# Kernel optimization log

Measured on AMD Instinct MI355X. Metric: run time of the kernel, lower is better.

## Reference

```python
import jax, jax.numpy as jnp
import numpy as np

N = 128       # SSM state size
L = 32768     # l_max / sequence length
DT_MIN, DT_MAX = 0.001, 0.1


def setup_inputs() -> dict:
    key = jax.random.key(0)
    ku, ka, kb, kc, ks = jax.random.split(key, 5)
    u = jax.random.normal(ku, (L,), dtype=jnp.float32)
    # lecun_normal: std = 1/sqrt(fan_in); shift A by -2I for stability over L powers
    A = jax.random.normal(ka, (N, N), dtype=jnp.float32) * (1.0 / np.sqrt(N)) - 2.0 * jnp.eye(N, dtype=jnp.float32)
    B = jax.random.normal(kb, (N, 1), dtype=jnp.float32)            # fan_in=1 -> std 1
    C = jax.random.normal(kc, (1, N), dtype=jnp.float32) * (1.0 / np.sqrt(N))
    D = jnp.ones((1,), dtype=jnp.float32)
    log_step = jax.random.uniform(ks, (1,), dtype=jnp.float32) * (np.log(DT_MAX) - np.log(DT_MIN)) + np.log(DT_MIN)
    return {"u": u, "A": A, "B": B, "C": C, "D": D, "log_step": log_step}


def discretize(a, b, step):
    # bilinear (Tustin) discretization, identical to the flax module
    i = jnp.eye(a.shape[0], dtype=a.dtype)
    bl = jnp.linalg.inv(i - (step / 2.0) * a)
    ab = bl @ (i + (step / 2.0) * a)
    bb = (bl * step) @ b
    return ab, bb


def k_conv(ab, bb, cb, l):
    # K[t] = cb @ ab^t @ bb  -- same math as the matrix_power list-comp,
    # computed with a single scan carrying x_t = ab^t @ bb  (N,1)
    def step(x, _):
        k_t = (cb @ x).reshape(())
        return ab @ x, k_t
    _, k = jax.lax.scan(step, bb, None, length=l)
    return k  # (l,)


def causal_convolution(u, k):
    l = u.shape[0]
    ud = jnp.fft.rfft(jnp.pad(u, (0, k.shape[0])))
    kd = jnp.fft.rfft(jnp.pad(k, (0, l)))
    return jnp.fft.irfft(ud * kd)[:l]


def reference(u, A, B, C, D, log_step):
    step = jnp.exp(log_step)
    ab, bb = discretize(A, B, step)
    K = k_conv(ab, bb, C, u.shape[0])
    return causal_convolution(u, K) + D * u
```

## Files before the change

### kernel.cpp

```cpp
#include <hip/hip_runtime.h>
#include <math.h>

#define L_SEQ 32768
#define PL 16384
#define PLG 32768

typedef unsigned short u16;
typedef float f32x4 __attribute__((ext_vector_type(4)));
typedef short bf16x8 __attribute__((ext_vector_type(8)));
typedef u16 u16x4 __attribute__((ext_vector_type(4)));

__device__ __forceinline__ u16 f2bf(float x) {
  unsigned u = __float_as_uint(x);
  u = u + 0x7FFFu + ((u >> 16) & 1u);
  return (u16)(u >> 16);
}
__device__ __forceinline__ float bf2f(u16 h) { return __uint_as_float(((unsigned)h) << 16); }
__device__ __forceinline__ int MIDX(int r, int c) { return (r << 7) + (c ^ ((r & 7) << 3)); }
__device__ __forceinline__ f32x4 MF(bf16x8 a, bf16x8 b, f32x4 c) {
  return __builtin_amdgcn_mfma_f32_16x16x32_bf16(a, b, c, 0, 0, 0);
}
__device__ __forceinline__ void gfrag(const u16* g, int row, int kp, bf16x8& h, bf16x8& l) {
  h = *(const bf16x8*)(g + row * 128 + kp);
  l = *(const bf16x8*)(g + PLG + row * 128 + kp);
}
__device__ __forceinline__ void lfrag(const u16* base, int row, int kp, bf16x8& h, bf16x8& l) {
  h = *(const bf16x8*)(base + MIDX(row, kp));
  l = *(const bf16x8*)(base + PL + MIDX(row, kp));
}
__device__ __forceinline__ void pack4(const float* v, u16x4& hi, u16x4& lo) {
#pragma unroll
  for (int j = 0; j < 4; ++j) {
    u16 h = f2bf(v[j]);
    hi[j] = h;
    lo[j] = f2bf(v[j] - bf2f(h));
  }
}

template<int MK, int ERS, bool HEC, bool M2, bool DUMP>
__device__ void step(u16* lds,
                     const u16* gAm, const u16* gU, float c3, u16* gDump,
                     int ER, const u16* gAe, u16* gOe, int eR0,
                     const u16* gT1, const u16* gT2x,
                     int EC, const u16* gBe, u16* gOc, int eC0) {
  u16* Mb = lds;
  u16* Tb = lds + 2 * PL;
  const int t = threadIdx.x, lane = t & 63, la = lane & 15, g = lane >> 4;
  const int w = t >> 6, wr = w >> 2, wc = w & 3;
  const int r0 = wr << 5, c0 = wc << 5;
  constexpr int ERN = (ERS > 0) ? ERS : 1;

  __syncthreads();

  f32x4 acc[2][2], accT[2][2], accE[ERN][2], accC[2][2];
#pragma unroll
  for (int i = 0; i < 2; ++i)
#pragma unroll
    for (int j = 0; j < 2; ++j) {
      acc[i][j] = (f32x4){0.f, 0.f, 0.f, 0.f};
      accT[i][j] = (f32x4){0.f, 0.f, 0.f, 0.f};
      accC[i][j] = (f32x4){0.f, 0.f, 0.f, 0.f};
    }
#pragma unroll
  for (int f = 0; f < ERN; ++f)
#pragma unroll
    for (int j = 0; j < 2; ++j) accE[f][j] = (f32x4){0.f, 0.f, 0.f, 0.f};

#pragma unroll
  for (int kb = 0; kb < 4; ++kb) {
    const int kp = (kb << 5) + (g << 3);
    bf16x8 Ah[2], Al[2], Bh[2], Bl[2];
    if constexpr (MK != 0) {
#pragma unroll
      for (int fr = 0; fr < 2; ++fr) {
        int ar = r0 + (fr << 4) + la;
        if constexpr (MK == 1) lfrag(Mb, ar, kp, Ah[fr], Al[fr]);
        else gfrag(gAm, ar, kp, Ah[fr], Al[fr]);
      }
    }
#pragma unroll
    for (int fc = 0; fc < 2; ++fc) {
      int bc = c0 + (fc << 4) + la;
      lfrag(Tb, bc, kp, Bh[fc], Bl[fc]);
    }
    bf16x8 Eh[ERN], El[ERN];
    if constexpr (ERS > 0) {
#pragma unroll
      for (int f = 0; f < ERS; ++f) {
        int er = (wr << 4) + (f << 6) + la;
        gfrag(gAe, er, kp, Eh[f], El[f]);
      }
    }
    bf16x8 Fh[2], Fl[2];
    if constexpr (HEC) {
#pragma unroll
      for (int e = 0; e < 2; ++e) {
        int ec = (wc << 5) + (e << 4) + la;
        gfrag(gBe, ec, kp, Fh[e], Fl[e]);
      }
    }
    if constexpr (MK != 0) {
#pragma unroll
      for (int fr = 0; fr < 2; ++fr)
#pragma unroll
        for (int fc = 0; fc < 2; ++fc) {
          acc[fr][fc] = MF(Ah[fr], Bh[fc], acc[fr][fc]);
          acc[fr][fc] = MF(Ah[fr], Bl[fc], acc[fr][fc]);
          acc[fr][fc] = MF(Al[fr], Bh[fc], acc[fr][fc]);
          accT[fr][fc] = MF(Bh[fc], Ah[fr], accT[fr][fc]);
          accT[fr][fc] = MF(Bh[fc], Al[fr], accT[fr][fc]);
          accT[fr][fc] = MF(Bl[fc], Ah[fr], accT[fr][fc]);
        }
    }
    if constexpr (ERS > 0) {
#pragma unroll
      for (int f = 0; f < ERS; ++f)
#pragma unroll
        for (int fc = 0; fc < 2; ++fc) {
          accE[f][fc] = MF(Bh[fc], Eh[f], accE[f][fc]);
          accE[f][fc] = MF(Bh[fc], El[f], accE[f][fc]);
          accE[f][fc] = MF(Bl[fc], Eh[f], accE[f][fc]);
        }
    }
    if constexpr (HEC) {
#pragma unroll
      for (int fr = 0; fr < 2; ++fr)
#pragma unroll
        for (int e = 0; e < 2; ++e) {
          accC[fr][e] = MF(Ah[fr], Fh[e], accC[fr][e]);
          accC[fr][e] = MF(Ah[fr], Fl[e], accC[fr][e]);
          accC[fr][e] = MF(Al[fr], Fh[e], accC[fr][e]);
        }
    }
  }

  __syncthreads();

  if constexpr (MK != 0) {
#pragma unroll
    for (int fr = 0; fr < 2; ++fr)
#pragma unroll
      for (int fc = 0; fc < 2; ++fc) {
        int rr = r0 + (fr << 4) + la;
        int cb = c0 + (fc << 4) + (g << 2);
        float v[4];
#pragma unroll
        for (int j = 0; j < 4; ++j) v[j] = accT[fr][fc][j];
        if constexpr (MK == 2) {
#pragma unroll
          for (int j = 0; j < 4; ++j)
            v[j] = c3 * (v[j] + bf2f(gU[rr * 128 + cb + j]) +
                         bf2f(gU[PLG + rr * 128 + cb + j])) -
                   ((rr == cb + j) ? 1.f : 0.f);
        }
        u16x4 hi, lo;
        pack4(v, hi, lo);
        *(u16x4*)(Mb + MIDX(rr, cb)) = hi;
        *(u16x4*)(Mb + PL + MIDX(rr, cb)) = lo;
        if constexpr (DUMP) {
          *(u16x4*)(gDump + rr * 128 + cb) = hi;
          *(u16x4*)(gDump + PLG + rr * 128 + cb) = lo;
        }
        int cc = c0 + (fc << 4) + la;
        int rb = r0 + (fr << 4) + (g << 2);
        float q[4];
#pragma unroll
        for (int j = 0; j < 4; ++j) q[j] = acc[fr][fc][j];
        if constexpr (MK == 2) {
#pragma unroll
          for (int j = 0; j < 4; ++j)
            q[j] = c3 * (q[j] + bf2f(gU[(rb + j) * 128 + cc]) +
                         bf2f(gU[PLG + (rb + j) * 128 + cc])) -
                   ((rb + j == cc) ? 1.f : 0.f);
        }
        u16x4 hi2, lo2;
        pack4(q, hi2, lo2);
        *(u16x4*)(Tb + MIDX(cc, rb)) = hi2;
        *(u16x4*)(Tb + PL + MIDX(cc, rb)) = lo2;
      }
  }
  if constexpr (ERS > 0) {
#pragma unroll
    for (int f = 0; f < ERS; ++f) {
      int er = (wr << 4) + (f << 6) + la;
      if (er < ER) {
#pragma unroll
        for (int fc = 0; fc < 2; ++fc) {
          int cb = c0 + (fc << 4) + (g << 2);
          float v[4];
#pragma unroll
          for (int j = 0; j < 4; ++j) v[j] = accE[f][fc][j];
          if constexpr (M2) {
            u16x4 t1h = *(const u16x4*)(gT1 + er * 128 + cb);
            u16x4 t1l = *(const u16x4*)(gT1 + PLG + er * 128 + cb);
            u16x4 t2h = *(const u16x4*)(gT2x + er * 128 + cb);
            u16x4 t2l = *(const u16x4*)(gT2x + PLG + er * 128 + cb);
#pragma unroll
            for (int j = 0; j < 4; ++j)
              v[j] += bf2f(t1h[j]) + bf2f(t1l[j]) + bf2f(t2h[j]) + bf2f(t2l[j]) +
                      ((er == cb + j) ? 1.f : 0.f);
          }
          u16x4 hi, lo;
          pack4(v, hi, lo);
          *(u16x4*)(gOe + (eR0 + er) * 128 + cb) = hi;
          *(u16x4*)(gOe + PLG + (eR0 + er) * 128 + cb) = lo;
        }
      }
    }
  }
  if constexpr (HEC) {
#pragma unroll
    for (int e = 0; e < 2; ++e) {
      int ec = (wc << 5) + (e << 4) + la;
      if (ec < EC) {
#pragma unroll
        for (int fr = 0; fr < 2; ++fr) {
          int rb = r0 + (fr << 4) + (g << 2);
          float v[4];
#pragma unroll
          for (int j = 0; j < 4; ++j) v[j] = accC[fr][e][j];
          u16x4 hi, lo;
          pack4(v, hi, lo);
          *(u16x4*)(gOc + (eC0 + ec) * 128 + rb) = hi;
          *(u16x4*)(gOc + PLG + (eC0 + ec) * 128 + rb) = lo;
        }
      }
    }
  }
}

__global__ void __launch_bounds__(1024)
__attribute__((amdgpu_waves_per_eu(1, 4)))
chain_k(const float* __restrict__ A, const float* __restrict__ Bv,
        const float* __restrict__ Cv, const float* __restrict__ lstep,
        u16* ws) {
  extern __shared__ u16 lds[];
  const int bid = blockIdx.x;
  u16* gT  = ws + bid * 98304;
  u16* gT2 = gT + 32768;
  u16* gU  = gT + 65536;
  u16* rt  = ws + 196608;
  u16* gs  = ws + 262144;

  const int t = threadIdx.x;
  const float stp = expf(lstep[0]);
  const float alpha = 0.5f * stp / (1.f + stp);
  const float c3 = 2.f / (1.f + stp);
  u16* Mh = lds; u16* Ml = lds + PL; u16* Th = lds + 2 * PL; u16* Tl = lds + 3 * PL;

#pragma unroll
  for (int i = 0; i < 4; ++i) {
    int e4 = (t + (i << 10)) << 2;
    int r = e4 >> 7, c = e4 & 127;
    float4 av = *(const float4*)(A + e4);
    float vv[4] = {av.x, av.y, av.z, av.w};
    float tv[4];
#pragma unroll
    for (int j = 0; j < 4; ++j) tv[j] = alpha * (vv[j] + ((r == c + j) ? 2.f : 0.f));
    u16x4 hi, lo;
    pack4(tv, hi, lo);
    *(u16x4*)(Mh + MIDX(r, c)) = hi;
    *(u16x4*)(Ml + MIDX(r, c)) = lo;
    *(u16x4*)(gT + r * 128 + c) = hi;
    *(u16x4*)(gT + PLG + r * 128 + c) = lo;
#pragma unroll
    for (int j = 0; j < 4; ++j) {
      Th[MIDX(c + j, r)] = hi[j];
      Tl[MIDX(c + j, r)] = lo[j];
    }
  }

  step<1,0,false,false,true>(lds, 0, 0, 0.f, gT2,
                             0, 0, 0, 0, 0, 0, 0, 0, 0, 0);
  step<1,2,false,true,false>(lds, 0, 0, 0.f, 0,
                             128, gT, gU, 0, gT, gT2, 0, 0, 0, 0);
  step<2,0,false,false,false>(lds, gU, gU, c3, 0,
                              0, 0, 0, 0, 0, 0, 0, 0, 0, 0);

  if (bid == 0) {
    __syncthreads();
    if (t < 128) {
      float a2 = 0.f;
      for (int p = 0; p < 128; ++p)
        a2 = fmaf(bf2f(Mh[MIDX(t, p)]) + bf2f(Ml[MIDX(t, p)]), Bv[p], a2);
      float v = 0.5f * stp * (a2 + Bv[t]);
      u16 h = f2bf(v);
      rt[t] = h;
      rt[PLG + t] = f2bf(v - bf2f(h));
    }
    for (int i = 1; i <= 8; ++i) {
      int EC = 1 << (i - 1);
      step<1,0,true,false,false>(lds, 0, 0, 0.f, 0,
                                 0, 0, 0, 0, 0, 0, EC, rt, rt, EC);
    }
  } else {
    __syncthreads();
    if (t < 128) {
      float v = Cv[t];
      u16 h = f2bf(v);
      gs[t] = h;
      gs[PLG + t] = f2bf(v - bf2f(h));
    }
    for (int i = 1; i <= 8; ++i)
      step<1,0,false,false,false>(lds, 0, 0, 0.f, 0,
                                  0, 0, 0, 0, 0, 0, 0, 0, 0, 0);
    for (int j = 0; j <= 5; ++j) {
      int ER = 1 << j;
      step<1,1,false,false,false>(lds, 0, 0, 0.f, 0,
                                  ER, gs, gs, ER, 0, 0, 0, 0, 0, 0);
    }
    step<0,1,false,false,false>(lds, 0, 0, 0.f, 0,
                                64, gs, gs, 64, 0, 0, 0, 0, 0, 0);
  }
}

__global__ __launch_bounds__(256) void kmat_k(const u16* __restrict__ gs,
                                              const u16* __restrict__ rt,
                                              float* __restrict__ Kv) {
  __shared__ float srow[128];
  int t1 = blockIdx.x, t0 = threadIdx.x;
  if (t0 < 128)
    srow[t0] = bf2f(gs[t1 * 128 + t0]) + bf2f(gs[PLG + t1 * 128 + t0]);
  __syncthreads();
  const u16* rh = rt + t0 * 128;
  const u16* rl = rt + PLG + t0 * 128;
  float acc = 0.f;
#pragma unroll 4
  for (int p = 0; p < 128; p += 8) {
    uint4 qh = *(const uint4*)(rh + p);
    uint4 ql = *(const uint4*)(rl + p);
    unsigned dh[4] = {qh.x, qh.y, qh.z, qh.w};
    unsigned dl[4] = {ql.x, ql.y, ql.z, ql.w};
#pragma unroll
    for (int j = 0; j < 4; ++j) {
      acc = fmaf(srow[p + 2 * j],     bf2f((u16)dh[j]) + bf2f((u16)dl[j]), acc);
      acc = fmaf(srow[p + 2 * j + 1],
                 bf2f((u16)(dh[j] >> 16)) + bf2f((u16)(dl[j] >> 16)), acc);
    }
  }
  Kv[t1 * 256 + t0] = acc;
}

__global__ __launch_bounds__(64) void conv_k(const float* __restrict__ u,
                                             const float* __restrict__ Kv,
                                             float* __restrict__ Pp) {
  __shared__ __align__(16) float ks[512];
  __shared__ __align__(16) float usw[1536];

  int bid = blockIdx.x, tid = threadIdx.x;
  int m = (int)((sqrtf(4.f * (float)bid + 1.f) - 1.f) * 0.5f);
  while ((m + 1) * (m + 2) <= bid) ++m;
  while (m * (m + 1) > bid) --m;
  int j = bid - m * (m + 1);
  int w0 = (m << 10) - (j << 9) - 512;

  for (int idx = tid; idx < 512; idx += 64) ks[idx] = Kv[(j << 9) + idx];
  for (int idx = tid; idx < 1536; idx += 64) {
    int gi = w0 + idx;
    float v = (gi >= 0) ? u[gi] : 0.f;
    int b = idx >> 2, pb = b ^ ((b >> 3) & 7);
    usw[(pb << 2) | (idx & 3)] = v;
  }
  __syncthreads();

  int tb = tid << 4;
  float acc[16];
#pragma unroll
  for (int z = 0; z < 16; ++z) acc[z] = 0.f;

#define LD4(x) (*(const float4*)&usw[((((x) >> 2) ^ ((((x) >> 2) >> 3) & 7)) << 2)])
  float wf[20];
  {
    float4 a0 = LD4(508 + tb), a1 = LD4(512 + tb), a2 = LD4(516 + tb),
           a3 = LD4(520 + tb), a4 = LD4(524 + tb);
    wf[0] = a0.x; wf[1] = a0.y; wf[2] = a0.z; wf[3] = a0.w;
    wf[4] = a1.x; wf[5] = a1.y; wf[6] = a1.z; wf[7] = a1.w;
    wf[8] = a2.x; wf[9] = a2.y; wf[10] = a2.z; wf[11] = a2.w;
    wf[12] = a3.x; wf[13] = a3.y; wf[14] = a3.z; wf[15] = a3.w;
    wf[16] = a4.x; wf[17] = a4.y; wf[18] = a4.z; wf[19] = a4.w;
  }
  for (int q = 0; q < 512; q += 4) {
    float4 k4 = *(const float4*)&ks[q];
    float kk[4] = {k4.x, k4.y, k4.z, k4.w};
#pragma unroll
    for (int ds = 0; ds < 4; ++ds)
#pragma unroll
      for (int oi = 0; oi < 16; ++oi)
        acc[oi] = fmaf(kk[ds], wf[oi - ds + 4], acc[oi]);
    if (q < 508) {
#pragma unroll
      for (int z = 19; z >= 4; --z) wf[z] = wf[z - 4];
      float4 nw = LD4(504 + tb - q);
      wf[0] = nw.x; wf[1] = nw.y; wf[2] = nw.z; wf[3] = nw.w;
    }
  }
#undef LD4

  float* dst = Pp + (bid << 10) + tb;
#pragma unroll
  for (int z = 0; z < 16; z += 4)
    *(float4*)(dst + z) = make_float4(acc[z], acc[z + 1], acc[z + 2], acc[z + 3]);
}

__global__ __launch_bounds__(256) void reduce_k(const float* __restrict__ Pp,
                                                const float* __restrict__ u,
                                                const float* __restrict__ D,
                                                float* __restrict__ y) {
  int t = blockIdx.x * 256 + threadIdx.x;
  if (t >= L_SEQ) return;
  int m = t >> 10;
  int nJ = 2 * (m + 1);
  const float* base = Pp + ((m * (m + 1)) << 10) + (t & 1023);
  float acc = D[0] * u[t];
  for (int j = 0; j < nJ; ++j) acc += base[j << 10];
  y[t] = acc;
}

extern "C" void kernel_launch(void* const* d_in, const int* in_sizes, int n_in,
                              void* d_out, int out_size, void* d_ws, size_t ws_size,
                              hipStream_t stream) {
  (void)in_sizes; (void)n_in; (void)out_size; (void)ws_size;
  const float* u     = (const float*)d_in[0];
  const float* A     = (const float*)d_in[1];
  const float* B     = (const float*)d_in[2];
  const float* C     = (const float*)d_in[3];
  const float* D     = (const float*)d_in[4];
  const float* lstep = (const float*)d_in[5];
  float* y = (float*)d_out;
  u16* ws = (u16*)d_ws;

  u16* rt = ws + 196608;
  u16* gs = ws + 262144;
  float* Kv = (float*)((char*)d_ws + 622592);
  float* Pp = (float*)((char*)d_ws + 753664);

  (void)hipFuncSetAttribute((const void*)chain_k,
                            hipFuncAttributeMaxDynamicSharedMemorySize, 131072);
  hipLaunchKernelGGL(chain_k, dim3(2), dim3(1024), 131072, stream, A, B, C, lstep, ws);
  hipLaunchKernelGGL(kmat_k, dim3(128), dim3(256), 0, stream, gs, rt, Kv);
  hipLaunchKernelGGL(conv_k, dim3(1056), dim3(64), 0, stream, u, Kv, Pp);
  hipLaunchKernelGGL(reduce_k, dim3(L_SEQ / 256), dim3(256), 0, stream, Pp, u, D, y);
}
```

Before: 236.7 us.

## Split matrix-power chain into producer block and two flag-synchronised consumer blocks

Before, two blocks each redundantly computed the Cayley inverse and the power chain, and each then ran its own doubling steps serially. Now one producer block computes the powers of the discretised matrix once and publishes each one to a global slot behind a release flag. Two consumer blocks spin on those flags and build the K-vector row and column tables as soon as each power is ready, so the doubling work overlaps with the chain. This adds inter-block spin-wait synchronisation, coherent atomic loads and stores, and a memset, and it assumes all three blocks are co-resident or it could deadlock.

Result: slower. 304.9 us (+28.8%).

```diff
diff --git a/kernel.cpp b/kernel.cpp
--- a/kernel.cpp
+++ b/kernel.cpp
@@ -2,8 +2,8 @@
 #include <math.h>
 
 #define L_SEQ 32768
-#define PL 16384
-#define PLG 32768
+#define PL  16384
+#define GPL 16384
 
 typedef unsigned short u16;
 typedef float f32x4 __attribute__((ext_vector_type(4)));
@@ -20,14 +20,6 @@
 __device__ __forceinline__ f32x4 MF(bf16x8 a, bf16x8 b, f32x4 c) {
   return __builtin_amdgcn_mfma_f32_16x16x32_bf16(a, b, c, 0, 0, 0);
 }
-__device__ __forceinline__ void gfrag(const u16* g, int row, int kp, bf16x8& h, bf16x8& l) {
-  h = *(const bf16x8*)(g + row * 128 + kp);
-  l = *(const bf16x8*)(g + PLG + row * 128 + kp);
-}
-__device__ __forceinline__ void lfrag(const u16* base, int row, int kp, bf16x8& h, bf16x8& l) {
-  h = *(const bf16x8*)(base + MIDX(row, kp));
-  l = *(const bf16x8*)(base + PL + MIDX(row, kp));
-}
 __device__ __forceinline__ void pack4(const float* v, u16x4& hi, u16x4& lo) {
 #pragma unroll
   for (int j = 0; j < 4; ++j) {
@@ -36,13 +28,52 @@
     lo[j] = f2bf(v[j] - bf2f(h));
   }
 }
-
-template<int MK, int ERS, bool HEC, bool M2, bool DUMP>
-__device__ void step(u16* lds,
-                     const u16* gAm, const u16* gU, float c3, u16* gDump,
-                     int ER, const u16* gAe, u16* gOe, int eR0,
-                     const u16* gT1, const u16* gT2x,
-                     int EC, const u16* gBe, u16* gOc, int eC0) {
+__device__ __forceinline__ void gfragP(const u16* g, int pl, int row, int kp,
+                                       bf16x8& h, bf16x8& l) {
+  h = *(const bf16x8*)(g + row * 128 + kp);
+  l = *(const bf16x8*)(g + pl + row * 128 + kp);
+}
+__device__ __forceinline__ bf16x8 cohld16(const u16* p) {
+  unsigned long long a = __hip_atomic_load((const unsigned long long*)p,
+                                           __ATOMIC_RELAXED, __HIP_MEMORY_SCOPE_AGENT);
+  unsigned long long b = __hip_atomic_load((const unsigned long long*)p + 1,
+                                           __ATOMIC_RELAXED, __HIP_MEMORY_SCOPE_AGENT);
+  union { unsigned long long x[2]; bf16x8 v; } u;
+  u.x[0] = a; u.x[1] = b;
+  return u.v;
+}
+__device__ __forceinline__ void gfragC(const u16* g, int row, int kp,
+                                       bf16x8& h, bf16x8& l) {
+  h = cohld16(g + row * 128 + kp);
+  l = cohld16(g + GPL + row * 128 + kp);
+}
+__device__ __forceinline__ void cohst8(u16* p, u16x4 v) {
+  union { u16x4 s; unsigned long long x; } u;
+  u.s = v;
+  __hip_atomic_store((unsigned long long*)p, u.x, __ATOMIC_RELAXED,
+                     __HIP_MEMORY_SCOPE_AGENT);
+}
+__device__ __forceinline__ void waitflag(int* f) {
+  if (threadIdx.x == 0) {
+    int it = 0;
+    while (__hip_atomic_load(f, __ATOMIC_ACQUIRE, __HIP_MEMORY_SCOPE_AGENT) == 0 &&
+           it < (1 << 28)) {
+      __builtin_amdgcn_s_sleep(8);
+      ++it;
+    }
+  }
+  __syncthreads();
+}
+__device__ __forceinline__ void setflag(int* f) {
+  __syncthreads();
+  if (threadIdx.x == 0)
+    __hip_atomic_store(f, 1, __ATOMIC_RELEASE, __HIP_MEMORY_SCOPE_AGENT);
+}
+
+template<int MK, int DMP, int ERS, bool M2>
+__device__ void prod_step(u16* lds, const u16* gA, const u16* gU, float c3,
+                          u16* gd, const u16* gAe, u16* gOe,
+                          const u16* gT1, const u16* gT2x) {
   u16* Mb = lds;
   u16* Tb = lds + 2 * PL;
   const int t = threadIdx.x, lane = t & 63, la = lane & 15, g = lane >> 4;
@@ -52,14 +83,13 @@
 
   __syncthreads();
 
-  f32x4 acc[2][2], accT[2][2], accE[ERN][2], accC[2][2];
+  f32x4 acc[2][2], accT[2][2], accE[ERN][2];
 #pragma unroll
   for (int i = 0; i < 2; ++i)
 #pragma unroll
     for (int j = 0; j < 2; ++j) {
       acc[i][j] = (f32x4){0.f, 0.f, 0.f, 0.f};
       accT[i][j] = (f32x4){0.f, 0.f, 0.f, 0.f};
-      accC[i][j] = (f32x4){0.f, 0.f, 0.f, 0.f};
     }
 #pragma unroll
   for (int f = 0; f < ERN; ++f)
@@ -70,48 +100,41 @@
   for (int kb = 0; kb < 4; ++kb) {
     const int kp = (kb << 5) + (g << 3);
     bf16x8 Ah[2], Al[2], Bh[2], Bl[2];
-    if constexpr (MK != 0) {
-#pragma unroll
-      for (int fr = 0; fr < 2; ++fr) {
-        int ar = r0 + (fr << 4) + la;
-        if constexpr (MK == 1) lfrag(Mb, ar, kp, Ah[fr], Al[fr]);
-        else gfrag(gAm, ar, kp, Ah[fr], Al[fr]);
+#pragma unroll
+    for (int fr = 0; fr < 2; ++fr) {
+      int ar = r0 + (fr << 4) + la;
+      if constexpr (MK == 1) {
+        Ah[fr] = *(const bf16x8*)(Mb + MIDX(ar, kp));
+        Al[fr] = *(const bf16x8*)(Mb + PL + MIDX(ar, kp));
+      } else {
+        gfragP(gA, GPL, ar, kp, Ah[fr], Al[fr]);
       }
     }
 #pragma unroll
     for (int fc = 0; fc < 2; ++fc) {
       int bc = c0 + (fc << 4) + la;
-      lfrag(Tb, bc, kp, Bh[fc], Bl[fc]);
+      Bh[fc] = *(const bf16x8*)(Tb + MIDX(bc, kp));
+      Bl[fc] = *(const bf16x8*)(Tb + PL + MIDX(bc, kp));
     }
     bf16x8 Eh[ERN], El[ERN];
     if constexpr (ERS > 0) {
 #pragma unroll
       for (int f = 0; f < ERS; ++f) {
         int er = (wr << 4) + (f << 6) + la;
-        gfrag(gAe, er, kp, Eh[f], El[f]);
-      }
-    }
-    bf16x8 Fh[2], Fl[2];
-    if constexpr (HEC) {
-#pragma unroll
-      for (int e = 0; e < 2; ++e) {
-        int ec = (wc << 5) + (e << 4) + la;
-        gfrag(gBe, ec, kp, Fh[e], Fl[e]);
-      }
-    }
-    if constexpr (MK != 0) {
-#pragma unroll
-      for (int fr = 0; fr < 2; ++fr)
-#pragma unroll
-        for (int fc = 0; fc < 2; ++fc) {
-          acc[fr][fc] = MF(Ah[fr], Bh[fc], acc[fr][fc]);
-          acc[fr][fc] = MF(Ah[fr], Bl[fc], acc[fr][fc]);
-          acc[fr][fc] = MF(Al[fr], Bh[fc], acc[fr][fc]);
-          accT[fr][fc] = MF(Bh[fc], Ah[fr], accT[fr][fc]);
-          accT[fr][fc] = MF(Bh[fc], Al[fr], accT[fr][fc]);
-          accT[fr][fc] = MF(Bl[fc], Ah[fr], accT[fr][fc]);
-        }
-    }
+        gfragP(gAe, GPL, er, kp, Eh[f], El[f]);
+      }
+    }
+#pragma unroll
+    for (int fr = 0; fr < 2; ++fr)
+#pragma unroll
+      for (int fc = 0; fc < 2; ++fc) {
+        acc[fr][fc] = MF(Ah[fr], Bh[fc], acc[fr][fc]);
+        acc[fr][fc] = MF(Ah[fr], Bl[fc], acc[fr][fc]);
+        acc[fr][fc] = MF(Al[fr], Bh[fc], acc[fr][fc]);
+        accT[fr][fc] = MF(Bh[fc], Ah[fr], accT[fr][fc]);
+        accT[fr][fc] = MF(Bh[fc], Al[fr], accT[fr][fc]);
+        accT[fr][fc] = MF(Bl[fc], Ah[fr], accT[fr][fc]);
+      }
     if constexpr (ERS > 0) {
 #pragma unroll
       for (int f = 0; f < ERS; ++f)
@@ -122,195 +145,275 @@
           accE[f][fc] = MF(Bl[fc], Eh[f], accE[f][fc]);
         }
     }
-    if constexpr (HEC) {
-#pragma unroll
-      for (int fr = 0; fr < 2; ++fr)
-#pragma unroll
-        for (int e = 0; e < 2; ++e) {
-          accC[fr][e] = MF(Ah[fr], Fh[e], accC[fr][e]);
-          accC[fr][e] = MF(Ah[fr], Fl[e], accC[fr][e]);
-          accC[fr][e] = MF(Al[fr], Fh[e], accC[fr][e]);
-        }
-    }
-  }
-
-  __syncthreads();
-
-  if constexpr (MK != 0) {
-#pragma unroll
-    for (int fr = 0; fr < 2; ++fr)
+  }
+
+  __syncthreads();
+
+#pragma unroll
+  for (int fr = 0; fr < 2; ++fr)
+#pragma unroll
+    for (int fc = 0; fc < 2; ++fc) {
+      int rr = r0 + (fr << 4) + la;
+      int cb = c0 + (fc << 4) + (g << 2);
+      float v[4];
+#pragma unroll
+      for (int j = 0; j < 4; ++j) v[j] = accT[fr][fc][j];
+      if constexpr (MK == 2) {
+#pragma unroll
+        for (int j = 0; j < 4; ++j)
+          v[j] = c3 * (v[j] + bf2f(gU[rr * 128 + cb + j]) +
+                       bf2f(gU[GPL + rr * 128 + cb + j])) -
+                 ((rr == cb + j) ? 1.f : 0.f);
+      }
+      u16x4 hi, lo;
+      pack4(v, hi, lo);
+      *(u16x4*)(Mb + MIDX(rr, cb)) = hi;
+      *(u16x4*)(Mb + PL + MIDX(rr, cb)) = lo;
+      if constexpr (DMP == 1) {
+        *(u16x4*)(gd + rr * 128 + cb) = hi;
+        *(u16x4*)(gd + GPL + rr * 128 + cb) = lo;
+      }
+      if constexpr (DMP == 2) {
+        cohst8(gd + rr * 128 + cb, hi);
+        cohst8(gd + GPL + rr * 128 + cb, lo);
+      }
+      int cc = c0 + (fc << 4) + la;
+      int rb = r0 + (fr << 4) + (g << 2);
+      float q[4];
+#pragma unroll
+      for (int j = 0; j < 4; ++j) q[j] = acc[fr][fc][j];
+      if constexpr (MK == 2) {
+#pragma unroll
+        for (int j = 0; j < 4; ++j)
+          q[j] = c3 * (q[j] + bf2f(gU[(rb + j) * 128 + cc]) +
+                       bf2f(gU[GPL + (rb + j) * 128 + cc])) -
+                 ((rb + j == cc) ? 1.f : 0.f);
+      }
+      u16x4 hi2, lo2;
+      pack4(q, hi2, lo2);
+      *(u16x4*)(Tb + MIDX(cc, rb)) = hi2;
+      *(u16x4*)(Tb + PL + MIDX(cc, rb)) = lo2;
+      if constexpr (DMP == 3) {
+        cohst8(gd + cc * 128 + rb, hi2);
+        cohst8(gd + GPL + cc * 128 + rb, lo2);
+      }
+    }
+  if constexpr (ERS > 0) {
+#pragma unroll
+    for (int f = 0; f < ERS; ++f) {
+      int er = (wr << 4) + (f << 6) + la;
 #pragma unroll
       for (int fc = 0; fc < 2; ++fc) {
-        int rr = r0 + (fr << 4) + la;
         int cb = c0 + (fc << 4) + (g << 2);
         float v[4];
 #pragma unroll
-        for (int j = 0; j < 4; ++j) v[j] = accT[fr][fc][j];
-        if constexpr (MK == 2) {
+        for (int j = 0; j < 4; ++j) v[j] = accE[f][fc][j];
+        if constexpr (M2) {
+          u16x4 t1h = *(const u16x4*)(gT1 + er * 128 + cb);
+          u16x4 t1l = *(const u16x4*)(gT1 + GPL + er * 128 + cb);
+          u16x4 t2h = *(const u16x4*)(gT2x + er * 128 + cb);
+          u16x4 t2l = *(const u16x4*)(gT2x + GPL + er * 128 + cb);
 #pragma unroll
           for (int j = 0; j < 4; ++j)
-            v[j] = c3 * (v[j] + bf2f(gU[rr * 128 + cb + j]) +
-                         bf2f(gU[PLG + rr * 128 + cb + j])) -
-                   ((rr == cb + j) ? 1.f : 0.f);
+            v[j] += bf2f(t1h[j]) + bf2f(t1l[j]) + bf2f(t2h[j]) + bf2f(t2l[j]) +
+                    ((er == cb + j) ? 1.f : 0.f);
         }
         u16x4 hi, lo;
         pack4(v, hi, lo);
-        *(u16x4*)(Mb + MIDX(rr, cb)) = hi;
-        *(u16x4*)(Mb + PL + MIDX(rr, cb)) = lo;
-        if constexpr (DUMP) {
-          *(u16x4*)(gDump + rr * 128 + cb) = hi;
-          *(u16x4*)(gDump + PLG + rr * 128 + cb) = lo;
-        }
-        int cc = c0 + (fc << 4) + la;
-        int rb = r0 + (fr << 4) + (g << 2);
-        float q[4];
-#pragma unroll
-        for (int j = 0; j < 4; ++j) q[j] = acc[fr][fc][j];
-        if constexpr (MK == 2) {
-#pragma unroll
-          for (int j = 0; j < 4; ++j)
-            q[j] = c3 * (q[j] + bf2f(gU[(rb + j) * 128 + cc]) +
-                         bf2f(gU[PLG + (rb + j) * 128 + cc])) -
-                   ((rb + j == cc) ? 1.f : 0.f);
-        }
-        u16x4 hi2, lo2;
-        pack4(q, hi2, lo2);
-        *(u16x4*)(Tb + MIDX(cc, rb)) = hi2;
-        *(u16x4*)(Tb + PL + MIDX(cc, rb)) = lo2;
-      }
-  }
-  if constexpr (ERS > 0) {
-#pragma unroll
-    for (int f = 0; f < ERS; ++f) {
-      int er = (wr << 4) + (f << 6) + la;
-      if (er < ER) {
-#pragma unroll
-        for (int fc = 0; fc < 2; ++fc) {
-          int cb = c0 + (fc << 4) + (g << 2);
-          float v[4];
-#pragma unroll
-          for (int j = 0; j < 4; ++j) v[j] = accE[f][fc][j];
-          if constexpr (M2) {
-            u16x4 t1h = *(const u16x4*)(gT1 + er * 128 + cb);
-            u16x4 t1l = *(const u16x4*)(gT1 + PLG + er * 128 + cb);
-            u16x4 t2h = *(const u16x4*)(gT2x + er * 128 + cb);
-            u16x4 t2l = *(const u16x4*)(gT2x + PLG + er * 128 + cb);
-#pragma unroll
-            for (int j = 0; j < 4; ++j)
-              v[j] += bf2f(t1h[j]) + bf2f(t1l[j]) + bf2f(t2h[j]) + bf2f(t2l[j]) +
-                      ((er == cb + j) ? 1.f : 0.f);
-          }
-          u16x4 hi, lo;
-          pack4(v, hi, lo);
-          *(u16x4*)(gOe + (eR0 + er) * 128 + cb) = hi;
-          *(u16x4*)(gOe + PLG + (eR0 + er) * 128 + cb) = lo;
-        }
-      }
-    }
-  }
-  if constexpr (HEC) {
+        *(u16x4*)(gOe + er * 128 + cb) = hi;
+        *(u16x4*)(gOe + GPL + er * 128 + cb) = lo;
+      }
+    }
+  }
+}
+
+__device__ void cons_rdbl(const u16* slot, u16* rt, int EC) {
+  const int t = threadIdx.x, lane = t & 63, la = lane & 15, g = lane >> 4;
+  const int w = t >> 6, wr = w >> 2, wc = w & 3;
+  const int r0 = wr << 5;
+  __syncthreads();
+
+  f32x4 accC[2][2];
+#pragma unroll
+  for (int i = 0; i < 2; ++i)
+#pragma unroll
+    for (int j = 0; j < 2; ++j) accC[i][j] = (f32x4){0.f, 0.f, 0.f, 0.f};
+
+#pragma unroll
+  for (int kb = 0; kb < 4; ++kb) {
+    const int kp = (kb << 5) + (g << 3);
+    bf16x8 Ah[2], Al[2], Fh[2], Fl[2];
+#pragma unroll
+    for (int fr = 0; fr < 2; ++fr) {
+      int ar = r0 + (fr << 4) + la;
+      gfragC(slot, ar, kp, Ah[fr], Al[fr]);
+    }
 #pragma unroll
     for (int e = 0; e < 2; ++e) {
       int ec = (wc << 5) + (e << 4) + la;
-      if (ec < EC) {
-#pragma unroll
-        for (int fr = 0; fr < 2; ++fr) {
-          int rb = r0 + (fr << 4) + (g << 2);
-          float v[4];
-#pragma unroll
-          for (int j = 0; j < 4; ++j) v[j] = accC[fr][e][j];
-          u16x4 hi, lo;
-          pack4(v, hi, lo);
-          *(u16x4*)(gOc + (eC0 + ec) * 128 + rb) = hi;
-          *(u16x4*)(gOc + PLG + (eC0 + ec) * 128 + rb) = lo;
-        }
-      }
-    }
-  }
-}
-
-__global__ void __launch_bounds__(1024)
-__attribute__((amdgpu_waves_per_eu(1, 4)))
-chain_k(const float* __restrict__ A, const float* __restrict__ Bv,
-        const float* __restrict__ Cv, const float* __restrict__ lstep,
-        u16* ws) {
+      gfragP(rt, 32768, ec, kp, Fh[e], Fl[e]);
+    }
+#pragma unroll
+    for (int fr = 0; fr < 2; ++fr)
+#pragma unroll
+      for (int e = 0; e < 2; ++e) {
+        accC[fr][e] = MF(Ah[fr], Fh[e], accC[fr][e]);
+        accC[fr][e] = MF(Ah[fr], Fl[e], accC[fr][e]);
+        accC[fr][e] = MF(Al[fr], Fh[e], accC[fr][e]);
+      }
+  }
+#pragma unroll
+  for (int e = 0; e < 2; ++e) {
+    int ec = ((t >> 6) & 3) * 32 + (e << 4) + la;
+    if (ec < EC) {
+#pragma unroll
+      for (int fr = 0; fr < 2; ++fr) {
+        int rb = r0 + (fr << 4) + (g << 2);
+        float v[4];
+#pragma unroll
+        for (int j = 0; j < 4; ++j) v[j] = accC[fr][e][j];
+        u16x4 hi, lo;
+        pack4(v, hi, lo);
+        *(u16x4*)(rt + (EC + ec) * 128 + rb) = hi;
+        *(u16x4*)(rt + 32768 + (EC + ec) * 128 + rb) = lo;
+      }
+    }
+  }
+  __syncthreads();
+}
+
+__device__ void cons_sdbl(const u16* slotT, u16* gs, int ER) {
+  const int t = threadIdx.x, lane = t & 63, la = lane & 15, g = lane >> 4;
+  const int w = t >> 6, wr = w >> 2, wc = w & 3;
+  const int c0 = wc << 5;
+  const int er = (wr << 4) + la;
+  __syncthreads();
+
+  f32x4 accE[2];
+#pragma unroll
+  for (int j = 0; j < 2; ++j) accE[j] = (f32x4){0.f, 0.f, 0.f, 0.f};
+
+#pragma unroll
+  for (int kb = 0; kb < 4; ++kb) {
+    const int kp = (kb << 5) + (g << 3);
+    bf16x8 Eh, El, Bh[2], Bl[2];
+    gfragP(gs, GPL, er, kp, Eh, El);
+#pragma unroll
+    for (int fc = 0; fc < 2; ++fc) {
+      int bc = c0 + (fc << 4) + la;
+      gfragC(slotT, bc, kp, Bh[fc], Bl[fc]);
+    }
+#pragma unroll
+    for (int fc = 0; fc < 2; ++fc) {
+      accE[fc] = MF(Bh[fc], Eh, accE[fc]);
+      accE[fc] = MF(Bh[fc], El, accE[fc]);
+      accE[fc] = MF(Bl[fc], Eh, accE[fc]);
+    }
+  }
+  if (er < ER) {
+#pragma unroll
+    for (int fc = 0; fc < 2; ++fc) {
+      int cb = c0 + (fc << 4) + (g << 2);
+      float v[4];
+#pragma unroll
+      for (int j = 0; j < 4; ++j) v[j] = accE[fc][j];
+      u16x4 hi, lo;
+      pack4(v, hi, lo);
+      *(u16x4*)(gs + (ER + er) * 128 + cb) = hi;
+      *(u16x4*)(gs + GPL + (ER + er) * 128 + cb) = lo;
+    }
+  }
+  __syncthreads();
+}
+
+__global__ void __launch_bounds__(1024) chain_k(const float* __restrict__ A,
+                                                const float* __restrict__ Bv,
+                                                const float* __restrict__ Cv,
+                                                const float* __restrict__ lstep,
+                                                u16* ws) {
   extern __shared__ u16 lds[];
-  const int bid = blockIdx.x;
-  u16* gT  = ws + bid * 98304;
-  u16* gT2 = gT + 32768;
-  u16* gU  = gT + 65536;
-  u16* rt  = ws + 196608;
-  u16* gs  = ws + 262144;
+  int* flags = (int*)ws;
+  u16* rt = ws + 512;
+  u16* gs = rt + 65536;
+  u16* scr = ws + 512 + 65536 + 32768 + 65536;
+  u16* gT = scr;
+  u16* gT2 = scr + 32768;
+  u16* gU = scr + 65536;
+  u16* slots = scr + 98304;
 
   const int t = threadIdx.x;
   const float stp = expf(lstep[0]);
   const float alpha = 0.5f * stp / (1.f + stp);
   const float c3 = 2.f / (1.f + stp);
-  u16* Mh = lds; u16* Ml = lds + PL; u16* Th = lds + 2 * PL; u16* Tl = lds + 3 * PL;
-
-#pragma unroll
-  for (int i = 0; i < 4; ++i) {
-    int e4 = (t + (i << 10)) << 2;
-    int r = e4 >> 7, c = e4 & 127;
-    float4 av = *(const float4*)(A + e4);
-    float vv[4] = {av.x, av.y, av.z, av.w};
-    float tv[4];
-#pragma unroll
-    for (int j = 0; j < 4; ++j) tv[j] = alpha * (vv[j] + ((r == c + j) ? 2.f : 0.f));
-    u16x4 hi, lo;
-    pack4(tv, hi, lo);
-    *(u16x4*)(Mh + MIDX(r, c)) = hi;
-    *(u16x4*)(Ml + MIDX(r, c)) = lo;
-    *(u16x4*)(gT + r * 128 + c) = hi;
-    *(u16x4*)(gT + PLG + r * 128 + c) = lo;
-#pragma unroll
-    for (int j = 0; j < 4; ++j) {
-      Th[MIDX(c + j, r)] = hi[j];
-      Tl[MIDX(c + j, r)] = lo[j];
-    }
-  }
-
-  step<1,0,false,false,true>(lds, 0, 0, 0.f, gT2,
-                             0, 0, 0, 0, 0, 0, 0, 0, 0, 0);
-  step<1,2,false,true,false>(lds, 0, 0, 0.f, 0,
-                             128, gT, gU, 0, gT, gT2, 0, 0, 0, 0);
-  step<2,0,false,false,false>(lds, gU, gU, c3, 0,
-                              0, 0, 0, 0, 0, 0, 0, 0, 0, 0);
-
-  if (bid == 0) {
-    __syncthreads();
+
+  if (blockIdx.x == 1) {
+    u16* Mh = lds; u16* Ml = lds + PL; u16* Th = lds + 2 * PL; u16* Tl = lds + 3 * PL;
+#pragma unroll
+    for (int i = 0; i < 4; ++i) {
+      int e4 = (t + (i << 10)) << 2;
+      int r = e4 >> 7, c = e4 & 127;
+      float4 av = *(const float4*)(A + e4);
+      float vv[4] = {av.x, av.y, av.z, av.w};
+      float tv[4];
+#pragma unroll
+      for (int j = 0; j < 4; ++j) tv[j] = alpha * (vv[j] + ((r == c + j) ? 2.f : 0.f));
+      u16x4 hi, lo;
+      pack4(tv, hi, lo);
+      *(u16x4*)(Mh + MIDX(r, c)) = hi;
+      *(u16x4*)(Ml + MIDX(r, c)) = lo;
+      *(u16x4*)(gT + r * 128 + c) = hi;
+      *(u16x4*)(gT + GPL + r * 128 + c) = lo;
+#pragma unroll
+      for (int j = 0; j < 4; ++j) {
+        Th[MIDX(c + j, r)] = hi[j];
+        Tl[MIDX(c + j, r)] = lo[j];
+      }
+    }
+    prod_step<1, 1, 0, false>(lds, 0, 0, 0.f, gT2, 0, 0, 0, 0);
+    prod_step<1, 0, 2, true>(lds, 0, 0, 0.f, 0, gT, gU, gT, gT2);
+    prod_step<2, 2, 0, false>(lds, gU, gU, c3, slots + 0, 0, 0, 0, 0);
+    setflag(flags + 0);
+    for (int k = 1; k <= 7; ++k) {
+      prod_step<1, 2, 0, false>(lds, 0, 0, 0.f, slots + k * 32768, 0, 0, 0, 0);
+      setflag(flags + k);
+    }
+    for (int k = 8; k <= 14; ++k) {
+      prod_step<1, 3, 0, false>(lds, 0, 0, 0.f, slots + k * 32768, 0, 0, 0, 0);
+      setflag(flags + k);
+    }
+  } else if (blockIdx.x == 0) {
+    waitflag(flags + 0);
     if (t < 128) {
       float a2 = 0.f;
-      for (int p = 0; p < 128; ++p)
-        a2 = fmaf(bf2f(Mh[MIDX(t, p)]) + bf2f(Ml[MIDX(t, p)]), Bv[p], a2);
+      const u16* s0 = slots;
+#pragma unroll 4
+      for (int p = 0; p < 128; p += 8) {
+        bf16x8 h = cohld16(s0 + t * 128 + p);
+        bf16x8 l = cohld16(s0 + GPL + t * 128 + p);
+#pragma unroll
+        for (int j = 0; j < 8; ++j)
+          a2 = fmaf(bf2f((u16)h[j]) + bf2f((u16)l[j]), Bv[p + j], a2);
+      }
       float v = 0.5f * stp * (a2 + Bv[t]);
       u16 h = f2bf(v);
       rt[t] = h;
-      rt[PLG + t] = f2bf(v - bf2f(h));
-    }
-    for (int i = 1; i <= 8; ++i) {
-      int EC = 1 << (i - 1);
-      step<1,0,true,false,false>(lds, 0, 0, 0.f, 0,
-                                 0, 0, 0, 0, 0, 0, EC, rt, rt, EC);
+      rt[32768 + t] = f2bf(v - bf2f(h));
+    }
+    for (int k = 0; k <= 7; ++k) {
+      if (k > 0) waitflag(flags + k);
+      cons_rdbl(slots + k * 32768, rt, 1 << k);
     }
   } else {
-    __syncthreads();
     if (t < 128) {
       float v = Cv[t];
       u16 h = f2bf(v);
       gs[t] = h;
-      gs[PLG + t] = f2bf(v - bf2f(h));
-    }
-    for (int i = 1; i <= 8; ++i)
-      step<1,0,false,false,false>(lds, 0, 0, 0.f, 0,
-                                  0, 0, 0, 0, 0, 0, 0, 0, 0, 0);
-    for (int j = 0; j <= 5; ++j) {
-      int ER = 1 << j;
-      step<1,1,false,false,false>(lds, 0, 0, 0.f, 0,
-                                  ER, gs, gs, ER, 0, 0, 0, 0, 0, 0);
-    }
-    step<0,1,false,false,false>(lds, 0, 0, 0.f, 0,
-                                64, gs, gs, 64, 0, 0, 0, 0, 0, 0);
+      gs[GPL + t] = f2bf(v - bf2f(h));
+    }
+    for (int j = 0; j <= 6; ++j) {
+      waitflag(flags + 8 + j);
+      cons_sdbl(slots + (8 + j) * 32768, gs, 1 << j);
+    }
   }
 }
 
@@ -320,10 +423,10 @@
   __shared__ float srow[128];
   int t1 = blockIdx.x, t0 = threadIdx.x;
   if (t0 < 128)
-    srow[t0] = bf2f(gs[t1 * 128 + t0]) + bf2f(gs[PLG + t1 * 128 + t0]);
+    srow[t0] = bf2f(gs[t1 * 128 + t0]) + bf2f(gs[GPL + t1 * 128 + t0]);
   __syncthreads();
   const u16* rh = rt + t0 * 128;
-  const u16* rl = rt + PLG + t0 * 128;
+  const u16* rl = rt + 32768 + t0 * 128;
   float acc = 0.f;
 #pragma unroll 4
   for (int p = 0; p < 128; p += 8) {
@@ -429,14 +532,15 @@
   float* y = (float*)d_out;
   u16* ws = (u16*)d_ws;
 
-  u16* rt = ws + 196608;
-  u16* gs = ws + 262144;
-  float* Kv = (float*)((char*)d_ws + 622592);
-  float* Pp = (float*)((char*)d_ws + 753664);
-
+  u16* rt = ws + 512;
+  u16* gs = ws + 66048;
+  float* Kv = (float*)((char*)d_ws + 197632);
+  float* Pp = (float*)((char*)d_ws + 328704);
+
+  hipMemsetAsync(d_ws, 0, 1024, stream);
   (void)hipFuncSetAttribute((const void*)chain_k,
                             hipFuncAttributeMaxDynamicSharedMemorySize, 131072);
-  hipLaunchKernelGGL(chain_k, dim3(2), dim3(1024), 131072, stream, A, B, C, lstep, ws);
+  hipLaunchKernelGGL(chain_k, dim3(3), dim3(1024), 131072, stream, A, B, C, lstep, ws);
   hipLaunchKernelGGL(kmat_k, dim3(128), dim3(256), 0, stream, gs, rt, Kv);
   hipLaunchKernelGGL(conv_k, dim3(1056), dim3(64), 0, stream, u, Kv, Pp);
   hipLaunchKernelGGL(reduce_k, dim3(L_SEQ / 256), dim3(256), 0, stream, Pp, u, D, y);
```
